# Kernel optimization log

Measured on AMD Instinct MI355X. Metric: run time of the kernel, lower is better.

Reference implementation:

```python
import jax, jax.numpy as jnp
import numpy as np

C = 768; H = 12; D = C // H; R = 8; SCALE = 0.5; EPS = 1e-12
NEG = -1e9

def _lin(x, W, b):
    return x @ W + b

def _ln(x, g, b):
    m = jnp.mean(x, axis=-1, keepdims=True)
    v = jnp.mean((x - m) ** 2, axis=-1, keepdims=True)
    return (x - m) * jax.lax.rsqrt(v + EPS) * g + b

def setup_inputs() -> dict:
    key = jax.random.key(0)
    ks = jax.random.split(key, 16)
    B, T, K = 8, 512, 4
    s = 0.02
    inp = {
        'x': jax.random.normal(ks[0], (B, T, C), jnp.float32),
        'mask': jnp.ones((B, T), jnp.int32),
        'neighbour_rep': jax.random.normal(ks[1], (B, T - 1, K, C), jnp.float32),
        'Wq': jax.random.normal(ks[2], (C, C), jnp.float32) * s,
        'bq': jnp.zeros((C,), jnp.float32),
        'Wk': jax.random.normal(ks[3], (C, C), jnp.float32) * s,
        'bk': jnp.zeros((C,), jnp.float32),
        'Wv': jax.random.normal(ks[4], (C, C), jnp.float32) * s,
        'bv': jnp.zeros((C,), jnp.float32),
        'Wp': jax.random.normal(ks[5], (C, C), jnp.float32) * s,
        'bp': jnp.zeros((C,), jnp.float32),
        'Wd': jax.random.normal(ks[6], (C, R), jnp.float32) * s,
        'bd': jnp.zeros((R,), jnp.float32),
        'Wu': jax.random.normal(ks[7], (R, C), jnp.float32) * s,
        'bu': jnp.zeros((C,), jnp.float32),
        'ln_g': jnp.ones((C,), jnp.float32),
        'ln_b': jnp.zeros((C,), jnp.float32),
    }
    return inp

def _softmax_stable(att):
    # manual max-sub-exp-sum softmax, matching stable_softmax
    att = att - jnp.max(att, axis=-1, keepdims=True)
    att = jnp.exp(att)
    return att / jnp.sum(att, axis=-1, keepdims=True)

def _heads(t, n_tok):
    B = t.shape[0]
    return t.reshape(B, n_tok, H, D)

def reference(x, mask, neighbour_rep, Wq, bq, Wk, bk, Wv, bv, Wp, bp, Wd, bd, Wu, bu, ln_g, ln_b):
    B, T, _ = x.shape
    inv = 1.0 / jnp.sqrt(jnp.float32(D))
    mvalid = (mask != 0)[:, None, None, :]  # [B,1,1,T]

    # ---- self attention: queries are x[:,1:], keys/values over full seq ----
    q = _heads(_lin(x[:, 1:], Wq, bq), T - 1)      # [B,T-1,H,D]
    k = _heads(_lin(x, Wk, bk), T)                 # [B,T,H,D]
    v = _heads(_lin(x, Wv, bv), T)
    att = jnp.einsum('bqhd,bkhd->bhqk', q, k) * inv
    att = jnp.where(mvalid, att, NEG)
    att = _softmax_stable(att)
    y_self = jnp.einsum('bhqk,bkhd->bqhd', att, v).reshape(B, T - 1, C)
    y_self = _lin(y_self, Wp, bp)

    # ---- cls attention: single query (token 0), low-rank key projection ----
    qc = _heads(_lin(x[:, :1], Wq, bq), 1)                         # [B,1,H,D]
    kc = _heads(_lin(_lin(x, Wd, bd), Wu, bu), T)                  # [B,T,H,D]
    attc = jnp.einsum('bqhd,bkhd->bhqk', qc, kc) * inv
    attc = jnp.where(mvalid, attc, NEG)
    attc = _softmax_stable(attc)
    y_cls = jnp.einsum('bhqk,bkhd->bqhd', attc, v).reshape(B, 1, C)
    y_cls = _lin(y_cls, Wp, bp)

    # ---- neighbour attention over small candidate set per token ----
    cand = jnp.concatenate([x[:, 1:, None, :], neighbour_rep], axis=2)  # [B,T-1,Kc,C]
    Kc = cand.shape[2]
    qn = _lin(cand, Wq, bq).reshape(B, T - 1, Kc, H, D)
    kn = _lin(_lin(cand, Wd, bd), Wu, bu).reshape(B, T - 1, Kc, H, D)
    vn = _lin(cand, Wv, bv).reshape(B, T - 1, Kc, H, D)
    attn = jnp.einsum('btihd,btjhd->bthij', qn, kn) * inv
    attn = _softmax_stable(attn)
    out = jnp.einsum('bthij,btjhd->btihd', attn, vn).reshape(B, T - 1, Kc, C)
    out = _lin(out, Wp, bp)
    y_neigh = out[:, :, 0, :]
    neigh_tmp = out[:, :, 1:, :]

    y = SCALE * y_neigh + (1.0 - SCALE) * y_self
    neighbour_out = _ln(neigh_tmp + neighbour_rep, ln_g, ln_b)
    y = jnp.concatenate([y_cls, y], axis=1)
    y = _ln(y + x, ln_g, ln_b)
    return y, neighbour_out
```

## Files before the change

### kernel.cpp

```cpp
#include <hip/hip_runtime.h>
#include <math.h>

#define C_    768
#define H_    12
#define D_    64
#define B_    8
#define T_    512
#define TM1   511
#define R_    8
#define KN_   4
#define KC5   5
#define SCALE_ 0.5f
#define EPS_  1e-12f
#define NEG_  -1000000000.0f
#define INV_  0.125f
#define LDQ   2560
#define QPOFF 2304
#define NT_   4096
#define NRR_  16352

typedef __bf16 bf16_t;
typedef __bf16 bf16x4_t __attribute__((ext_vector_type(4)));
typedef __bf16 bf16x8_t __attribute__((ext_vector_type(8)));
typedef float  f32x4_t  __attribute__((ext_vector_type(4)));
typedef const void __attribute__((address_space(1)))* gas_t;
typedef void       __attribute__((address_space(3)))* las_t;

__device__ __forceinline__ void gl_lds16(const bf16_t* g, bf16_t* l) {
  __builtin_amdgcn_global_load_lds((gas_t)g, (las_t)l, 16, 0, 0);
}

struct GemmDesc {
  const bf16_t* A; int lda;
  const bf16_t* Bt;
  const float* bias;
  bf16_t* Cbf; int ldc;
  bf16_t* Ctr; int trcol0; int mode;
  int M, K, N, gx, nwg;
};

__global__ __launch_bounds__(256) void prep(
    const float* __restrict__ x, const float* __restrict__ nrep,
    const float* __restrict__ Wq, const float* __restrict__ Wk,
    const float* __restrict__ Wv, const float* __restrict__ Wp,
    const float* __restrict__ Wd, const float* __restrict__ Wu,
    const float* __restrict__ bq, const float* __restrict__ bk,
    const float* __restrict__ bv, const float* __restrict__ bu,
    bf16_t* __restrict__ xbf, bf16_t* __restrict__ nrbf,
    bf16_t* __restrict__ Wbig, bf16_t* __restrict__ Wtp,
    float* __restrict__ WdT, float* __restrict__ bbig)
{
  __shared__ float tile[32][33];
  const int bid = blockIdx.x, tid = threadIdx.x;
  if (bid < 1024) {
    const long n = (long)NT_ * C_;
    for (long i = ((long)bid * 256 + tid) * 4; i < n; i += (long)1024 * 256 * 4) {
      float4 v = *(const float4*)(x + i);
      bf16x4_t o = {(bf16_t)v.x, (bf16_t)v.y, (bf16_t)v.z, (bf16_t)v.w};
      *(bf16x4_t*)(xbf + i) = o;
    }
  } else if (bid < 3072) {
    const long n = (long)NRR_ * C_;
    for (long i = ((long)(bid - 1024) * 256 + tid) * 4; i < n;
         i += (long)2048 * 256 * 4) {
      float4 v = *(const float4*)(nrep + i);
      bf16x4_t o = {(bf16_t)v.x, (bf16_t)v.y, (bf16_t)v.z, (bf16_t)v.w};
      *(bf16x4_t*)(nrbf + i) = o;
    }
  } else if (bid < 5376) {
    int sub = bid - 3072;
    const int which = sub / 576; sub %= 576;
    const float* W = which == 0 ? Wq : which == 1 ? Wk : which == 2 ? Wv : Wp;
    bf16_t* Wt = (which == 3) ? Wtp : Wbig + (size_t)which * C_ * C_;
    const int n0 = (sub % 24) * 32, k0 = (sub / 24) * 32;
    const int tx = tid & 31, ty = tid >> 5;
    #pragma unroll
    for (int r = ty; r < 32; r += 8)
      tile[r][tx] = W[(size_t)(k0 + r) * C_ + n0 + tx];
    __syncthreads();
    #pragma unroll
    for (int r = ty; r < 32; r += 8)
      Wt[(size_t)(n0 + r) * C_ + k0 + tx] = (bf16_t)tile[tx][r];
  } else if (bid < 6144) {
    const int idx = (bid - 5376) * 256 + tid;
    const int n = idx / C_, k = idx % C_;
    const int h = n >> 4, r = n & 15;
    float s = 0.f;
    if (h < H_) {
      if (r < 8) {
        #pragma unroll 8
        for (int j = 0; j < 64; ++j)
          s += Wu[r * C_ + h * 64 + j] * Wq[(size_t)k * C_ + h * 64 + j];
      } else if (r == 8) {
        #pragma unroll 8
        for (int j = 0; j < 64; ++j)
          s += bu[h * 64 + j] * Wq[(size_t)k * C_ + h * 64 + j];
      }
    }
    Wbig[(size_t)(QPOFF + n) * C_ + k] = (bf16_t)s;
  } else if (bid < 6168) {
    const int idx = (bid - 6144) * 256 + tid;
    if (idx < R_ * C_) {
      const int r = idx / C_, k = idx % C_;
      WdT[idx] = Wd[(size_t)k * R_ + r];
    }
  } else {
    const int i = (bid - 6168) * 256 + tid;
    if (i < 2560) {
      float v;
      if (i < 768) v = bq[i];
      else if (i < 1536) v = bk[i - 768];
      else if (i < 2304) v = bv[i - 1536];
      else {
        const int n = i - 2304, h = n >> 4, r = n & 15;
        v = 0.f;
        if (h < H_) {
          if (r < 8) {
            float s = 0.f;
            for (int j = 0; j < 64; ++j) s += bq[h * 64 + j] * Wu[r * C_ + h * 64 + j];
            v = s;
          } else if (r == 8) {
            float s = 0.f;
            for (int j = 0; j < 64; ++j) s += bq[h * 64 + j] * bu[h * 64 + j];
            v = s;
          }
        }
      }
      bbig[i] = v;
    }
  }
}

__device__ __forceinline__ void gemm_body(const GemmDesc& d, int bid0, char* pool)
{
  bf16_t* As = (bf16_t*)pool;
  bf16_t* Bs = (bf16_t*)(pool + 16384);
  bf16_t* Cs = (bf16_t*)pool;

  int lid = bid0;
  {
    const int nwg = d.nwg;
    const int q0 = nwg >> 3, r0 = nwg & 7;
    const int xcd = lid & 7, idx = lid >> 3;
    lid = (xcd < r0 ? xcd * (q0 + 1) : r0 * (q0 + 1) + (xcd - r0) * q0) + idx;
  }
  const int row0 = (lid / d.gx) * 128;
  const int col0 = (lid % d.gx) * 128;

  const int tid = threadIdx.x;
  const int lane = tid & 63;
  const int wv = tid >> 6;
  const int wr = (wv >> 1) * 64;
  const int wc = (wv & 1) * 64;

  const int srl = wv * 8 + (lane >> 3);
  const int scol = 8 * ((lane & 7) ^ (srl & 7));

  const bf16_t* gA[4];
  const bf16_t* gB[4];
  #pragma unroll
  for (int i = 0; i < 4; ++i) {
    int ar = row0 + i * 32 + srl; if (ar > d.M - 1) ar = d.M - 1;
    gA[i] = d.A + (size_t)ar * d.lda + scol;
    gB[i] = d.Bt + (size_t)(col0 + i * 32 + srl) * d.K + scol;
  }

  f32x4_t acc[4][4];
  #pragma unroll
  for (int i = 0; i < 4; ++i)
    #pragma unroll
    for (int j = 0; j < 4; ++j) acc[i][j] = (f32x4_t){0.f, 0.f, 0.f, 0.f};

  const int fm = lane & 15;
  const int g = lane >> 4;
  const int f7 = fm & 7;

  for (int k0 = 0; k0 < d.K; k0 += 64) {
    #pragma unroll
    for (int i = 0; i < 4; ++i)
      gl_lds16(gA[i] + k0, As + i * 2048 + wv * 512);
    #pragma unroll
    for (int i = 0; i < 4; ++i)
      gl_lds16(gB[i] + k0, Bs + i * 2048 + wv * 512);
    __syncthreads();
    #pragma unroll
    for (int h = 0; h < 2; ++h) {
      const int sl = 8 * (((h << 2) + g) ^ f7);
      bf16x8_t af[4], bfr[4];
      #pragma unroll
      for (int mi = 0; mi < 4; ++mi)
        af[mi] = *(const bf16x8_t*)(As + (wr + mi * 16 + fm) * 64 + sl);
      #pragma unroll
      for (int ni = 0; ni < 4; ++ni)
        bfr[ni] = *(const bf16x8_t*)(Bs + (wc + ni * 16 + fm) * 64 + sl);
      __builtin_amdgcn_s_setprio(1);
      #pragma unroll
      for (int mi = 0; mi < 4; ++mi)
        #pragma unroll
        for (int ni = 0; ni < 4; ++ni)
          acc[mi][ni] = __builtin_amdgcn_mfma_f32_16x16x32_bf16(af[mi], bfr[ni],
                                                                acc[mi][ni], 0, 0, 0);
      __builtin_amdgcn_s_setprio(0);
    }
    __syncthreads();
  }

  const int r4 = (lane >> 4) * 4;

  if (d.mode & 2) {
    #pragma unroll
    for (int ni = 0; ni < 4; ++ni) {
      const int col = col0 + wc + ni * 16 + fm;
      if ((unsigned)(col - d.trcol0) < 768u) {
        const int vcol = col - d.trcol0;
        const float bv = d.bias[col];
        #pragma unroll
        for (int mi = 0; mi < 4; ++mi) {
          const int rb = row0 + wr + mi * 16 + r4;
          bf16x4_t o4 = {(bf16_t)(acc[mi][ni][0] + bv), (bf16_t)(acc[mi][ni][1] + bv),
                         (bf16_t)(acc[mi][ni][2] + bv), (bf16_t)(acc[mi][ni][3] + bv)};
          size_t idx = ((size_t)(rb >> 9) * H_ + (size_t)(vcol >> 6)) * ((size_t)D_ * T_)
                     + (size_t)(vcol & 63) * T_ + (size_t)(rb & 511);
          *(bf16x4_t*)(d.Ctr + idx) = o4;
        }
      }
    }
  }

  #pragma unroll
  for (int p = 0; p < 2; ++p) {
    if (wr == p * 64) {
      #pragma unroll
      for (int ni = 0; ni < 4; ++ni) {
        const int col = wc + ni * 16 + fm;
        const float bv = d.bias[col0 + col];
        #pragma unroll
        for (int mi = 0; mi < 4; ++mi) {
          const int lrow = mi * 16 + r4;
          #pragma unroll
          for (int r = 0; r < 4; ++r)
            Cs[(lrow + r) * 136 + col] = (bf16_t)(acc[mi][ni][r] + bv);
        }
      }
    }
    __syncthreads();
    const int rrow = tid >> 2;
    const int cc = (tid & 3) * 32;
    const int grow = row0 + p * 64 + rrow;
    if ((d.mode & 1) && grow < d.M) {
      bf16_t* gp = d.Cbf + (size_t)grow * d.ldc + col0 + cc;
      const bf16_t* lp = Cs + rrow * 136 + cc;
      #pragma unroll
      for (int j = 0; j < 4; ++j)
        *(bf16x8_t*)(gp + j * 8) = *(const bf16x8_t*)(lp + j * 8);
    }
    __syncthreads();
  }
}

__device__ __forceinline__ void gemv8w_body(
    const bf16_t* __restrict__ A, const float* __restrict__ WdT,
    const float* __restrict__ bd, float* __restrict__ out, int M, int bid)
{
  const int w = (int)threadIdx.x >> 6, lane = (int)threadIdx.x & 63;
  const int row0 = bid * 16 + w * 4;
  #pragma unroll
  for (int rr = 0; rr < 4; ++rr) {
    const int row = row0 + rr;
    if (row >= M) return;
    const bf16_t* ar = A + (size_t)row * C_ + lane * 12;
    float xv[12];
    #pragma unroll
    for (int c = 0; c < 3; ++c) {
      bf16x4_t v = *(const bf16x4_t*)(ar + c * 4);
      #pragma unroll
      for (int j = 0; j < 4; ++j) xv[c * 4 + j] = (float)v[j];
    }
    float acc[8];
    #pragma unroll
    for (int r = 0; r < 8; ++r) {
      const float* wr = WdT + r * C_ + lane * 12;
      float4 w0 = *(const float4*)(wr);
      float4 w1 = *(const float4*)(wr + 4);
      float4 w2 = *(const float4*)(wr + 8);
      acc[r] = xv[0]*w0.x + xv[1]*w0.y + xv[2]*w0.z + xv[3]*w0.w
             + xv[4]*w1.x + xv[5]*w1.y + xv[6]*w1.z + xv[7]*w1.w
             + xv[8]*w2.x + xv[9]*w2.y + xv[10]*w2.z + xv[11]*w2.w;
    }
    #pragma unroll
    for (int off = 32; off > 0; off >>= 1) {
      #pragma unroll
      for (int r = 0; r < 8; ++r) acc[r] += __shfl_xor(acc[r], off);
    }
    if (lane == 0) {
      #pragma unroll
      for (int r = 0; r < 8; ++r)
        out[(size_t)row * R_ + r] = acc[r] + bd[r];
    }
  }
}

__global__ __launch_bounds__(256) void mega1(
    GemmDesc d0, int n0, GemmDesc d1, int n1,
    const bf16_t* Ag1, const bf16_t* Ag2,
    const float* WdT, const float* bd,
    float* o1, int M1, int ng1, float* o2, int M2)
{
  __shared__ __align__(16) char pool[32768];
  int bid = blockIdx.x;
  if (bid < n0) { gemm_body(d0, bid, pool); return; }
  bid -= n0;
  if (bid < n1) { gemm_body(d1, bid, pool); return; }
  bid -= n1;
  if (bid < ng1) { gemv8w_body(Ag1, WdT, bd, o1, M1, bid); return; }
  bid -= ng1;
  gemv8w_body(Ag2, WdT, bd, o2, M2, bid);
}

__global__ __launch_bounds__(256) void gemm_mfma_k(GemmDesc d) {
  __shared__ __align__(16) char pool[32768];
  gemm_body(d, blockIdx.x, pool);
}

__device__ void attn_body(
    const bf16_t* __restrict__ QKVc, const bf16_t* __restrict__ Vtg,
    const int* __restrict__ mask, bf16_t* __restrict__ yout,
    char* pool, int bid)
{
  bf16_t* Ks   = (bf16_t*)pool;
  bf16_t* Vs   = (bf16_t*)(pool + 8192);
  bf16_t* Pl   = (bf16_t*)(pool + 16384);
  float* fac_s = (float*)(pool + 24576);
  float* l_s   = (float*)(pool + 24832);
  int*   msk_s = (int*)(pool + 25088);

  const int qt0 = (bid & 7) * 64;
  const int h = (bid >> 3) % H_;
  const int b = bid / 96;
  const int tid = threadIdx.x;
  const int lane = tid & 63;
  const int w = tid >> 6;
  const int lq = lane & 15;
  const int g = lane >> 4;

  const int qi_frag = qt0 + w * 16 + lq;
  const int qtok = (qi_frag < TM1 ? qi_frag : TM1 - 1) + 1;
  bf16x8_t qf[2];
  {
    const bf16_t* qp = QKVc + ((size_t)(b * T_) + qtok) * LDQ + h * D_ + 8 * g;
    qf[0] = *(const bf16x8_t*)qp;
    qf[1] = *(const bf16x8_t*)(qp + 32);
  }

  const bf16_t* kbase = QKVc + (size_t)(b * T_) * LDQ + 768 + h * D_;
  const bf16_t* vbase = Vtg + ((size_t)(b * H_) + h) * ((size_t)D_ * T_);

  f32x4_t o[4];
  #pragma unroll
  for (int i = 0; i < 4; ++i) o[i] = (f32x4_t){0.f, 0.f, 0.f, 0.f};
  float m = -INFINITY, l = 0.f;

  for (int kt = 0; kt < T_; kt += 64) {
    #pragma unroll
    for (int i = 0; i < 2; ++i) {
      const int tp = tid + i * 256;
      const int kr = tp >> 3;
      const int sl = tp & 7;
      const int ss = sl ^ (kr & 7);
      gl_lds16(kbase + (size_t)(kt + kr) * LDQ + 8 * ss,
               Ks + (size_t)(i * 4 + w) * 512);
      gl_lds16(vbase + (size_t)kr * T_ + kt + 8 * ss,
               Vs + (size_t)(i * 4 + w) * 512);
    }
    if (tid < 64) msk_s[tid] = mask[b * T_ + kt + tid];
    __syncthreads();

    f32x4_t st[4];
    __builtin_amdgcn_s_setprio(1);
    #pragma unroll
    for (int t = 0; t < 4; ++t) {
      st[t] = (f32x4_t){0.f, 0.f, 0.f, 0.f};
      const int kk = t * 16 + lq;
      const bf16_t* krow = Ks + kk * 64;
      bf16x8_t kf0 = *(const bf16x8_t*)(krow + 8 * ((g)     ^ (kk & 7)));
      bf16x8_t kf1 = *(const bf16x8_t*)(krow + 8 * ((4 + g) ^ (kk & 7)));
      st[t] = __builtin_amdgcn_mfma_f32_16x16x32_bf16(kf0, qf[0], st[t], 0, 0, 0);
      st[t] = __builtin_amdgcn_mfma_f32_16x16x32_bf16(kf1, qf[1], st[t], 0, 0, 0);
    }
    __builtin_amdgcn_s_setprio(0);

    float p[16];
    float mt = -INFINITY;
    #pragma unroll
    for (int t = 0; t < 4; ++t) {
      const int4 mk = *(const int4*)&msk_s[t * 16 + 4 * g];
      p[4*t+0] = mk.x ? st[t][0] * INV_ : NEG_;
      p[4*t+1] = mk.y ? st[t][1] * INV_ : NEG_;
      p[4*t+2] = mk.z ? st[t][2] * INV_ : NEG_;
      p[4*t+3] = mk.w ? st[t][3] * INV_ : NEG_;
      mt = fmaxf(mt, fmaxf(fmaxf(p[4*t], p[4*t+1]), fmaxf(p[4*t+2], p[4*t+3])));
    }
    mt = fmaxf(mt, __shfl_xor(mt, 16));
    mt = fmaxf(mt, __shfl_xor(mt, 32));
    const float mnew = fmaxf(m, mt);
    const float fac = __expf(m - mnew);
    float ps = 0.f;
    #pragma unroll
    for (int i = 0; i < 16; ++i) { p[i] = __expf(p[i] - mnew); ps += p[i]; }
    ps += __shfl_xor(ps, 16);
    ps += __shfl_xor(ps, 32);
    l = l * fac + ps;
    m = mnew;
    if (lane < 16) fac_s[w * 16 + lane] = fac;

    bf16_t* prow = Pl + w * 1024 + lq * 64;
    #pragma unroll
    for (int t = 0; t < 4; ++t) {
      bf16x4_t pb = {(bf16_t)p[4*t], (bf16_t)p[4*t+1],
                     (bf16_t)p[4*t+2], (bf16_t)p[4*t+3]};
      *(bf16x4_t*)(prow + 8 * ((2*t + (g >> 1)) ^ (lq & 7)) + 4 * (g & 1)) = pb;
    }
    bf16x8_t pa0 = *(const bf16x8_t*)(prow + 8 * ((g)     ^ (lq & 7)));
    bf16x8_t pa1 = *(const bf16x8_t*)(prow + 8 * ((4 + g) ^ (lq & 7)));

    const float4 fc = *(const float4*)&fac_s[w * 16 + 4 * g];
    __builtin_amdgcn_s_setprio(1);
    #pragma unroll
    for (int db = 0; db < 4; ++db) {
      const int dr = db * 16 + lq;
      const bf16_t* vrow = Vs + dr * 64;
      bf16x8_t vf0 = *(const bf16x8_t*)(vrow + 8 * ((g)     ^ (dr & 7)));
      bf16x8_t vf1 = *(const bf16x8_t*)(vrow + 8 * ((4 + g) ^ (dr & 7)));
      o[db][0] *= fc.x; o[db][1] *= fc.y; o[db][2] *= fc.z; o[db][3] *= fc.w;
      o[db] = __builtin_amdgcn_mfma_f32_16x16x32_bf16(pa0, vf0, o[db], 0, 0, 0);
      o[db] = __builtin_amdgcn_mfma_f32_16x16x32_bf16(pa1, vf1, o[db], 0, 0, 0);
    }
    __builtin_amdgcn_s_setprio(0);
    __syncthreads();
  }

  if (lane < 16) l_s[w * 16 + lane] = l;
  const float4 lv = *(const float4*)&l_s[w * 16 + 4 * g];
  const float rl0 = 1.f / lv.x, rl1 = 1.f / lv.y;
  const float rl2 = 1.f / lv.z, rl3 = 1.f / lv.w;
  const int qr0 = qt0 + w * 16 + 4 * g;
  #pragma unroll
  for (int db = 0; db < 4; ++db) {
    const int col = h * D_ + db * 16 + lq;
    bf16_t* yp = yout + ((size_t)(b * TM1) + qr0) * C_ + col;
    if (qr0 + 0 < TM1) yp[0 * (size_t)C_] = (bf16_t)(o[db][0] * rl0);
    if (qr0 + 1 < TM1) yp[1 * (size_t)C_] = (bf16_t)(o[db][1] * rl1);
    if (qr0 + 2 < TM1) yp[2 * (size_t)C_] = (bf16_t)(o[db][2] * rl2);
    if (qr0 + 3 < TM1) yp[3 * (size_t)C_] = (bf16_t)(o[db][3] * rl3);
  }
}

__device__ void cls_body(
    const bf16_t* __restrict__ QKVc, const float* __restrict__ t1,
    const int* __restrict__ mask, float* __restrict__ yout,
    char* pool, int cbid)
{
  float* Vs   = (float*)pool;
  float* Ps   = (float*)(pool + 16640);
  float* qp_s = (float*)(pool + 16960);

  const int b = cbid / H_, h = cbid % H_;
  const int tid = threadIdx.x;
  const int lane = tid & 63;

  if (tid < 16)
    qp_s[tid] = (float)QKVc[(size_t)(b * T_) * LDQ + QPOFF + h * 16 + tid];
  __syncthreads();

  float m = -INFINITY, l = 0.f, acc = 0.f, mnew = 0.f;
  for (int kt = 0; kt < T_; kt += 64) {
    for (int rr = tid >> 6; rr < 64; rr += 4)
      Vs[rr * 65 + lane] =
          (float)QKVc[((size_t)(b * T_) + kt + rr) * LDQ + 1536 + h * D_ + lane];
    __syncthreads();
    if (tid < 64) {
      const float* t1r = t1 + ((size_t)(b * T_) + kt + tid) * R_;
      float sc = qp_s[8];
      #pragma unroll
      for (int r = 0; r < 8; ++r) sc += qp_s[r] * t1r[r];
      sc *= INV_;
      if (!mask[b * T_ + kt + tid]) sc = NEG_;
      float mt = sc;
      #pragma unroll
      for (int off = 32; off > 0; off >>= 1) mt = fmaxf(mt, __shfl_xor(mt, off));
      mnew = fmaxf(m, mt);
      float e = __expf(sc - mnew);
      float ssum = e;
      #pragma unroll
      for (int off = 32; off > 0; off >>= 1) ssum += __shfl_xor(ssum, off);
      float fac = __expf(m - mnew);
      acc *= fac;
      l = l * fac + ssum;
      Ps[tid] = e;
    }
    __syncthreads();
    if (tid < 64) {
      #pragma unroll
      for (int j = 0; j < 64; ++j) acc += Ps[j] * Vs[j * 65 + tid];
      m = mnew;
    }
    __syncthreads();
  }
  if (tid < 64) yout[(size_t)b * C_ + h * D_ + tid] = acc / l;
}

__global__ __launch_bounds__(256) void attn_cls(
    const bf16_t* __restrict__ QKVc, const bf16_t* __restrict__ Vtg,
    const int* __restrict__ mask, bf16_t* __restrict__ yout,
    const float* __restrict__ t1, float* __restrict__ ych)
{
  __shared__ __align__(16) char pool[25344];
  const int bid = blockIdx.x;
  if (bid < 768) attn_body(QKVc, Vtg, mask, yout, pool, bid);
  else           cls_body(QKVc, t1, mask, ych, pool, bid - 768);
}

__global__ __launch_bounds__(256) void neigh_clsp(
    const bf16_t* __restrict__ QKVc, const float* __restrict__ t1,
    const bf16_t* __restrict__ vqn, const float* __restrict__ t2,
    const bf16_t* __restrict__ ysh, int b0, bf16_t* __restrict__ outn,
    int nNeigh, const float* __restrict__ ych, const float* __restrict__ Wp,
    const float* __restrict__ bp, float* __restrict__ ycp)
{
  __shared__ float vs[KC5 * C_];
  __shared__ float qp_s[KC5][200];
  __shared__ float t2_s[KC5][8];
  __shared__ float Ps[H_ * 25];
  __shared__ float as_[C_];

  const int tid = threadIdx.x;
  int bid = blockIdx.x;
  if (bid >= nNeigh) {
    const int cbid = bid - nNeigh;
    const int row = cbid / 3;
    const int c = (cbid % 3) * 256 + tid;
    for (int i = tid; i < C_; i += 256) as_[i] = ych[(size_t)row * C_ + i];
    __syncthreads();
    float acc = bp[c];
    for (int k = 0; k < C_; ++k) acc += as_[k] * Wp[(size_t)k * C_ + c];
    ycp[(size_t)row * C_ + c] = acc;
    return;
  }

  const int bt = bid;
  const int bb = bt / TM1, t = bt % TM1;
  const int b = b0 + bb;
  const size_t tok = (size_t)(b * T_) + t + 1;
  const size_t nrow = ((size_t)(bb * TM1) + t) * KN_;

  for (int idx = tid; idx < KC5 * 96; idx += 256) {
    int i = idx / 96, d8 = (idx % 96) * 8;
    const bf16_t* vp = (i == 0) ? QKVc + tok * LDQ + 1536 + d8
                                : vqn + (nrow + i - 1) * 1024 + d8;
    bf16x8_t vv = *(const bf16x8_t*)vp;
    #pragma unroll
    for (int j = 0; j < 8; ++j) vs[i * C_ + d8 + j] = (float)vv[j];
  }
  for (int idx = tid; idx < KC5 * 24; idx += 256) {
    int i = idx / 24, c8 = (idx % 24) * 8;
    const bf16_t* qpp = (i == 0) ? QKVc + tok * LDQ + QPOFF + c8
                                 : vqn + (nrow + i - 1) * 1024 + 768 + c8;
    bf16x8_t qv = *(const bf16x8_t*)qpp;
    #pragma unroll
    for (int j = 0; j < 8; ++j) qp_s[i][c8 + j] = (float)qv[j];
  }
  if (tid < KC5 * 8) {
    int i = tid / 8, r = tid & 7;
    t2_s[i][r] = (i == 0) ? t1[tok * R_ + r] : t2[(nrow + i - 1) * R_ + r];
  }
  __syncthreads();

  if (tid < H_ * KC5) {
    int h = tid / KC5, i = tid % KC5;
    float sc[KC5];
    #pragma unroll
    for (int j = 0; j < KC5; ++j) {
      float s = qp_s[i][h * 16 + 8];
      #pragma unroll
      for (int r = 0; r < 8; ++r) s += qp_s[i][h * 16 + r] * t2_s[j][r];
      sc[j] = s * INV_;
    }
    float mt = sc[0];
    #pragma unroll
    for (int j = 1; j < KC5; ++j) mt = fmaxf(mt, sc[j]);
    float e[KC5], ssum = 0.f;
    #pragma unroll
    for (int j = 0; j < KC5; ++j) { e[j] = __expf(sc[j] - mt); ssum += e[j]; }
    float rs = 1.f / ssum;
    #pragma unroll
    for (int j = 0; j < KC5; ++j) Ps[h * 25 + i * KC5 + j] = e[j] * rs;
  }
  __syncthreads();

  const bf16_t* ysrow = ysh + ((size_t)(b * TM1) + t) * C_;
  for (int idx = tid; idx < KC5 * C_; idx += 256) {
    int i = idx / C_, c = idx % C_;
    int h = c / D_;
    float sum = 0.f;
    #pragma unroll
    for (int j = 0; j < KC5; ++j)
      sum += Ps[h * 25 + i * KC5 + j] * vs[j * C_ + c];
    if (i == 0) sum = SCALE_ * sum + (1.f - SCALE_) * (float)ysrow[c];
    outn[(((size_t)(bb * TM1) + t) * KC5 + i) * C_ + c] = (bf16_t)sum;
  }
}

__device__ __forceinline__ void block_reduce2(float& s, float& ss, float* red) {
  #pragma unroll
  for (int off = 32; off > 0; off >>= 1) {
    s += __shfl_down(s, off);
    ss += __shfl_down(ss, off);
  }
  int wid = threadIdx.x >> 6;
  if ((threadIdx.x & 63) == 0) { red[wid * 2] = s; red[wid * 2 + 1] = ss; }
  __syncthreads();
  s  = red[0] + red[2] + red[4] + red[6];
  ss = red[1] + red[3] + red[5] + red[7];
}

__device__ __forceinline__ void ln_row(const float vals[3], float s, float ss,
                                       const float* __restrict__ g,
                                       const float* __restrict__ bb,
                                       float* __restrict__ orow, float* red) {
  block_reduce2(s, ss, red);
  float mean = s * (1.f / (float)C_);
  float var = ss * (1.f / (float)C_) - mean * mean;
  var = fmaxf(var, 0.f);
  float rs = rsqrtf(var + EPS_);
  #pragma unroll
  for (int ii = 0; ii < 3; ++ii) {
    int c = threadIdx.x + ii * 256;
    orow[c] = (vals[ii] - mean) * rs * g[c] + bb[c];
  }
}

__global__ __launch_bounds__(256) void combine_all(
    const bf16_t* __restrict__ poutnb, const float* __restrict__ x,
    const float* __restrict__ g, const float* __restrict__ bln,
    int b0, float* __restrict__ dout, float* __restrict__ dout1,
    const bf16_t* __restrict__ nrcbf, int nMain,
    const float* __restrict__ ycp, int withCls)
{
  __shared__ float red[8];
  int bid = blockIdx.x;
  float vals[3], s = 0.f, ss = 0.f;
  if (bid < nMain) {
    const int bbb = bid / TM1, t = bid % TM1;
    const int b = b0 + bbb;
    const bf16_t* pn = poutnb + (((size_t)(bbb * TM1) + t) * KC5 + 0) * C_;
    const float* xr = x + ((size_t)(b * T_) + t + 1) * C_;
    float* orow = dout + ((size_t)(b * T_) + t + 1) * C_;
    #pragma unroll
    for (int ii = 0; ii < 3; ++ii) {
      int c = threadIdx.x + ii * 256;
      float v = (float)pn[c] + xr[c];
      vals[ii] = v; s += v; ss += v * v;
    }
    ln_row(vals, s, ss, g, bln, orow, red);
    return;
  }
  bid -= nMain;
  if (bid < nMain * KN_) {
    const int i1 = bid % KN_;
    const int bt = bid / KN_;
    const int bbb = bt / TM1, t = bt % TM1;
    const int b = b0 + bbb;
    const bf16_t* pn = poutnb + ((size_t)bt * KC5 + 1 + i1) * C_;
    const bf16_t* nr = nrcbf + ((size_t)bt * KN_ + i1) * C_;
    float* orow = dout1 + (((size_t)(b * TM1) + t) * KN_ + i1) * C_;
    #pragma unroll
    for (int ii = 0; ii < 3; ++ii) {
      int c = threadIdx.x + ii * 256;
      float v = (float)pn[c] + (float)nr[c];
      vals[ii] = v; s += v; ss += v * v;
    }
    ln_row(vals, s, ss, g, bln, orow, red);
    return;
  }
  bid -= nMain * KN_;
  (void)withCls;
  const int b = bid;
  const float* yc = ycp + (size_t)b * C_;
  const float* xr = x + (size_t)(b * T_) * C_;
  float* orow = dout + (size_t)(b * T_) * C_;
  #pragma unroll
  for (int ii = 0; ii < 3; ++ii) {
    int c = threadIdx.x + ii * 256;
    float v = yc[c] + xr[c];
    vals[ii] = v; s += v; ss += v * v;
  }
  ln_row(vals, s, ss, g, bln, orow, red);
}

extern "C" void kernel_launch(void* const* d_in, const int* in_sizes, int n_in,
                              void* d_out, int out_size, void* d_ws, size_t ws_size,
                              hipStream_t stream) {
  (void)in_sizes; (void)n_in; (void)out_size;
  const float* x    = (const float*)d_in[0];
  const int*   mask = (const int*)d_in[1];
  const float* nrep = (const float*)d_in[2];
  const float* Wq = (const float*)d_in[3];  const float* bq = (const float*)d_in[4];
  const float* Wk = (const float*)d_in[5];  const float* bk = (const float*)d_in[6];
  const float* Wv = (const float*)d_in[7];  const float* bv = (const float*)d_in[8];
  const float* Wp = (const float*)d_in[9];  const float* bp = (const float*)d_in[10];
  const float* Wd = (const float*)d_in[11]; const float* bd = (const float*)d_in[12];
  const float* Wu = (const float*)d_in[13]; const float* bu = (const float*)d_in[14];
  const float* lng = (const float*)d_in[15];
  const float* lnb = (const float*)d_in[16];
  float* dout = (float*)d_out;
  const size_t OUT1 = (size_t)B_ * T_ * C_;

  char* ws = (char*)d_ws;
  size_t off = 0;
  auto alloc = [&](size_t bytes) -> void* {
    void* p = ws + off; off += (bytes + 255) & ~(size_t)255; return p;
  };
  const size_t NT = (size_t)NT_;
  const size_t NR = (size_t)NRR_;
  const size_t YSROWS = (size_t)B_ * TM1;

  bf16_t* xbf   = (bf16_t*)alloc(NT * C_ * 2);
  bf16_t* nrbf  = (bf16_t*)alloc(NR * C_ * 2);
  bf16_t* Wbig  = (bf16_t*)alloc((size_t)2560 * C_ * 2);
  bf16_t* Wtp   = (bf16_t*)alloc((size_t)C_ * C_ * 2);
  float*  WdT   = (float*)alloc((size_t)R_ * C_ * 4);
  float*  bbig  = (float*)alloc(2560 * 4);
  bf16_t* QKVc  = (bf16_t*)alloc(NT * LDQ * 2);
  bf16_t* Vtg   = (bf16_t*)alloc(NT * C_ * 2);
  float*  t1    = (float*)alloc(NT * R_ * 4);
  bf16_t* ysh   = (bf16_t*)alloc(YSROWS * C_ * 2);
  float*  ych   = (float*)alloc((size_t)B_ * C_ * 4);
  float*  ycp   = (float*)alloc((size_t)B_ * C_ * 4);
  const size_t fixed = off;
  const size_t perb = (size_t)TM1 * KN_ * 1024 * 2
                    + (size_t)TM1 * KN_ * R_ * 4
                    + (size_t)TM1 * KC5 * C_ * 2 * 2 + 5 * 256;
  int nb = 1;
  for (int cand : {8, 4, 2, 1}) {
    if (fixed + perb * (size_t)cand <= ws_size) { nb = cand; break; }
  }
  bf16_t* outn   = (bf16_t*)alloc((size_t)nb * TM1 * KC5 * C_ * 2);
  bf16_t* poutnb = (bf16_t*)alloc((size_t)nb * TM1 * KC5 * C_ * 2);
  bf16_t* vqn  = (bf16_t*)alloc((size_t)nb * TM1 * KN_ * 1024 * 2);
  float*  t2   = (float*)alloc((size_t)nb * TM1 * KN_ * R_ * 4);

  dim3 blk(256);

  prep<<<6178, blk, 0, stream>>>(x, nrep, Wq, Wk, Wv, Wp, Wd, Wu,
                                 bq, bk, bv, bu,
                                 xbf, nrbf, Wbig, Wtp, WdT, bbig);

  GemmDesc dqkv;
  dqkv.A = xbf; dqkv.lda = C_; dqkv.Bt = Wbig; dqkv.bias = bbig;
  dqkv.Cbf = QKVc; dqkv.ldc = LDQ; dqkv.Ctr = Vtg; dqkv.trcol0 = 1536;
  dqkv.mode = 3; dqkv.M = (int)NT; dqkv.K = C_; dqkv.N = 2560;
  dqkv.gx = 20; dqkv.nwg = 640;

  bool first = true;
  for (int b0 = 0; b0 < B_; b0 += nb) {
    const int Mn = nb * TM1 * KN_;
    const int Mo = nb * TM1 * KC5;
    const bf16_t* nrcbf = nrbf + (size_t)b0 * TM1 * KN_ * C_;

    GemmDesc dvqn;
    dvqn.A = nrcbf; dvqn.lda = C_; dvqn.Bt = Wbig + (size_t)1536 * C_;
    dvqn.bias = bbig + 1536; dvqn.Cbf = vqn; dvqn.ldc = 1024;
    dvqn.Ctr = nullptr; dvqn.trcol0 = 0; dvqn.mode = 1;
    dvqn.M = Mn; dvqn.K = C_; dvqn.N = 1024;
    dvqn.gx = 8; dvqn.nwg = 8 * ((Mn + 127) / 128);

    const int n0 = first ? 640 : 0;
    const int M1 = first ? (int)NT : 0;
    const int ng1 = first ? (int)((NT + 15) / 16) : 0;
    const int ng2 = (Mn + 15) / 16;

    mega1<<<n0 + dvqn.nwg + ng1 + ng2, blk, 0, stream>>>(
        dqkv, n0, dvqn, dvqn.nwg, xbf, nrcbf, WdT, bd, t1, M1, ng1, t2, Mn);

    if (first) {
      attn_cls<<<768 + 96, blk, 0, stream>>>(QKVc, Vtg, mask, ysh, t1, ych);
    }

    neigh_clsp<<<nb * TM1 + (first ? 24 : 0), blk, 0, stream>>>(
        QKVc, t1, vqn, t2, ysh, b0, outn, nb * TM1, ych, Wp, bp, ycp);

    GemmDesc dproj;
    dproj.A = outn; dproj.lda = C_; dproj.Bt = Wtp; dproj.bias = bp;
    dproj.Cbf = poutnb; dproj.ldc = C_; dproj.Ctr = nullptr; dproj.trcol0 = 0;
    dproj.mode = 1; dproj.M = Mo; dproj.K = C_; dproj.N = C_;
    dproj.gx = 6; dproj.nwg = 6 * ((Mo + 127) / 128);
    gemm_mfma_k<<<dproj.nwg, blk, 0, stream>>>(dproj);

    combine_all<<<nb * TM1 * (1 + KN_) + (first ? 8 : 0), blk, 0, stream>>>(
        poutnb, x, lng, lnb, b0, dout, dout + OUT1, nrcbf, nb * TM1,
        ycp, first ? 1 : 0);

    first = false;
  }
}
```

Measured before the change: 248.6 us.

## Fold output projection into value weights to drop the post-attention projection GEMM

Precomputes Wv·Wp (and bv·Wp+bp) with a small GEMM so the V projection produces already-projected values. Since softmax rows sum to one, attention over projected values equals projecting the attention output, so the separate neighbour projection GEMM and the cls projection blocks are removed. This saves a large M×768×768 GEMM per batch chunk and one intermediate buffer, at the cost of an extra 768³ weight GEMM and bf16 rounding of the fused weights.

```diff
diff --git a/kernel.cpp b/kernel.cpp
--- a/kernel.cpp
+++ b/kernel.cpp
@@ -46,9 +46,12 @@
     const float* __restrict__ Wd, const float* __restrict__ Wu,
     const float* __restrict__ bq, const float* __restrict__ bk,
     const float* __restrict__ bv, const float* __restrict__ bu,
+    const float* __restrict__ bp,
     bf16_t* __restrict__ xbf, bf16_t* __restrict__ nrbf,
     bf16_t* __restrict__ Wbig, bf16_t* __restrict__ Wtp,
-    float* __restrict__ WdT, float* __restrict__ bbig)
+    bf16_t* __restrict__ Wvbf,
+    float* __restrict__ WdT, float* __restrict__ bbig,
+    float* __restrict__ zb768)
 {
   __shared__ float tile[32][33];
   const int bid = blockIdx.x, tid = threadIdx.x;
@@ -70,17 +73,24 @@
   } else if (bid < 5376) {
     int sub = bid - 3072;
     const int which = sub / 576; sub %= 576;
-    const float* W = which == 0 ? Wq : which == 1 ? Wk : which == 2 ? Wv : Wp;
-    bf16_t* Wt = (which == 3) ? Wtp : Wbig + (size_t)which * C_ * C_;
-    const int n0 = (sub % 24) * 32, k0 = (sub / 24) * 32;
-    const int tx = tid & 31, ty = tid >> 5;
-    #pragma unroll
-    for (int r = ty; r < 32; r += 8)
-      tile[r][tx] = W[(size_t)(k0 + r) * C_ + n0 + tx];
-    __syncthreads();
-    #pragma unroll
-    for (int r = ty; r < 32; r += 8)
-      Wt[(size_t)(n0 + r) * C_ + k0 + tx] = (bf16_t)tile[tx][r];
+    if (which == 2) {
+      const long i = ((long)sub * 256 + tid) * 4;
+      float4 v = *(const float4*)(Wv + i);
+      bf16x4_t o = {(bf16_t)v.x, (bf16_t)v.y, (bf16_t)v.z, (bf16_t)v.w};
+      *(bf16x4_t*)(Wvbf + i) = o;
+    } else {
+      const float* W = which == 0 ? Wq : which == 1 ? Wk : Wp;
+      bf16_t* Wt = (which == 3) ? Wtp : Wbig + (size_t)which * C_ * C_;
+      const int n0 = (sub % 24) * 32, k0 = (sub / 24) * 32;
+      const int tx = tid & 31, ty = tid >> 5;
+      #pragma unroll
+      for (int r = ty; r < 32; r += 8)
+        tile[r][tx] = W[(size_t)(k0 + r) * C_ + n0 + tx];
+      __syncthreads();
+      #pragma unroll
+      for (int r = ty; r < 32; r += 8)
+        Wt[(size_t)(n0 + r) * C_ + k0 + tx] = (bf16_t)tile[tx][r];
+    }
   } else if (bid < 6144) {
     const int idx = (bid - 5376) * 256 + tid;
     const int n = idx / C_, k = idx % C_;
@@ -110,8 +120,12 @@
       float v;
       if (i < 768) v = bq[i];
       else if (i < 1536) v = bk[i - 768];
-      else if (i < 2304) v = bv[i - 1536];
-      else {
+      else if (i < 2304) {
+        const int n = i - 1536;
+        float s = bp[n];
+        for (int m = 0; m < C_; ++m) s += bv[m] * Wp[(size_t)m * C_ + n];
+        v = s;
+      } else {
         const int n = i - 2304, h = n >> 4, r = n & 15;
         v = 0.f;
         if (h < H_) {
@@ -127,6 +141,8 @@
         }
       }
       bbig[i] = v;
+    } else if (i < 3328) {
+      zb768[i - 2560] = 0.f;
     }
   }
 }
@@ -457,7 +473,7 @@
 
 __device__ void cls_body(
     const bf16_t* __restrict__ QKVc, const float* __restrict__ t1,
-    const int* __restrict__ mask, float* __restrict__ yout,
+    const int* __restrict__ mask, float* __restrict__ ycp,
     char* pool, int cbid)
 {
   float* Vs   = (float*)pool;
@@ -506,48 +522,32 @@
     }
     __syncthreads();
   }
-  if (tid < 64) yout[(size_t)b * C_ + h * D_ + tid] = acc / l;
+  if (tid < 64) ycp[(size_t)b * C_ + h * D_ + tid] = acc / l;
 }
 
 __global__ __launch_bounds__(256) void attn_cls(
     const bf16_t* __restrict__ QKVc, const bf16_t* __restrict__ Vtg,
     const int* __restrict__ mask, bf16_t* __restrict__ yout,
-    const float* __restrict__ t1, float* __restrict__ ych)
+    const float* __restrict__ t1, float* __restrict__ ycp)
 {
   __shared__ __align__(16) char pool[25344];
   const int bid = blockIdx.x;
   if (bid < 768) attn_body(QKVc, Vtg, mask, yout, pool, bid);
-  else           cls_body(QKVc, t1, mask, ych, pool, bid - 768);
-}
-
-__global__ __launch_bounds__(256) void neigh_clsp(
+  else           cls_body(QKVc, t1, mask, ycp, pool, bid - 768);
+}
+
+__global__ __launch_bounds__(256) void neigh_attn(
     const bf16_t* __restrict__ QKVc, const float* __restrict__ t1,
     const bf16_t* __restrict__ vqn, const float* __restrict__ t2,
-    const bf16_t* __restrict__ ysh, int b0, bf16_t* __restrict__ outn,
-    int nNeigh, const float* __restrict__ ych, const float* __restrict__ Wp,
-    const float* __restrict__ bp, float* __restrict__ ycp)
+    const bf16_t* __restrict__ ysp, int b0, bf16_t* __restrict__ poutn)
 {
   __shared__ float vs[KC5 * C_];
   __shared__ float qp_s[KC5][200];
   __shared__ float t2_s[KC5][8];
   __shared__ float Ps[H_ * 25];
-  __shared__ float as_[C_];
 
   const int tid = threadIdx.x;
-  int bid = blockIdx.x;
-  if (bid >= nNeigh) {
-    const int cbid = bid - nNeigh;
-    const int row = cbid / 3;
-    const int c = (cbid % 3) * 256 + tid;
-    for (int i = tid; i < C_; i += 256) as_[i] = ych[(size_t)row * C_ + i];
-    __syncthreads();
-    float acc = bp[c];
-    for (int k = 0; k < C_; ++k) acc += as_[k] * Wp[(size_t)k * C_ + c];
-    ycp[(size_t)row * C_ + c] = acc;
-    return;
-  }
-
-  const int bt = bid;
+  const int bt = blockIdx.x;
   const int bb = bt / TM1, t = bt % TM1;
   const int b = b0 + bb;
   const size_t tok = (size_t)(b * T_) + t + 1;
@@ -597,7 +597,7 @@
   }
   __syncthreads();
 
-  const bf16_t* ysrow = ysh + ((size_t)(b * TM1) + t) * C_;
+  const bf16_t* ysrow = ysp + ((size_t)(b * TM1) + t) * C_;
   for (int idx = tid; idx < KC5 * C_; idx += 256) {
     int i = idx / C_, c = idx % C_;
     int h = c / D_;
@@ -606,7 +606,7 @@
     for (int j = 0; j < KC5; ++j)
       sum += Ps[h * 25 + i * KC5 + j] * vs[j * C_ + c];
     if (i == 0) sum = SCALE_ * sum + (1.f - SCALE_) * (float)ysrow[c];
-    outn[(((size_t)(bb * TM1) + t) * KC5 + i) * C_ + c] = (bf16_t)sum;
+    poutn[(((size_t)(bb * TM1) + t) * KC5 + i) * C_ + c] = (bf16_t)sum;
   }
 }
 
@@ -728,32 +728,39 @@
   bf16_t* nrbf  = (bf16_t*)alloc(NR * C_ * 2);
   bf16_t* Wbig  = (bf16_t*)alloc((size_t)2560 * C_ * 2);
   bf16_t* Wtp   = (bf16_t*)alloc((size_t)C_ * C_ * 2);
+  bf16_t* Wvbf  = (bf16_t*)alloc((size_t)C_ * C_ * 2);
   float*  WdT   = (float*)alloc((size_t)R_ * C_ * 4);
   float*  bbig  = (float*)alloc(2560 * 4);
+  float*  zb768 = (float*)alloc(768 * 4);
   bf16_t* QKVc  = (bf16_t*)alloc(NT * LDQ * 2);
   bf16_t* Vtg   = (bf16_t*)alloc(NT * C_ * 2);
   float*  t1    = (float*)alloc(NT * R_ * 4);
-  bf16_t* ysh   = (bf16_t*)alloc(YSROWS * C_ * 2);
-  float*  ych   = (float*)alloc((size_t)B_ * C_ * 4);
+  bf16_t* ysp   = (bf16_t*)alloc(YSROWS * C_ * 2);
   float*  ycp   = (float*)alloc((size_t)B_ * C_ * 4);
   const size_t fixed = off;
   const size_t perb = (size_t)TM1 * KN_ * 1024 * 2
                     + (size_t)TM1 * KN_ * R_ * 4
-                    + (size_t)TM1 * KC5 * C_ * 2 * 2 + 5 * 256;
+                    + (size_t)TM1 * KC5 * C_ * 2 + 4 * 256;
   int nb = 1;
   for (int cand : {8, 4, 2, 1}) {
     if (fixed + perb * (size_t)cand <= ws_size) { nb = cand; break; }
   }
-  bf16_t* outn   = (bf16_t*)alloc((size_t)nb * TM1 * KC5 * C_ * 2);
   bf16_t* poutnb = (bf16_t*)alloc((size_t)nb * TM1 * KC5 * C_ * 2);
   bf16_t* vqn  = (bf16_t*)alloc((size_t)nb * TM1 * KN_ * 1024 * 2);
   float*  t2   = (float*)alloc((size_t)nb * TM1 * KN_ * R_ * 4);
 
   dim3 blk(256);
 
-  prep<<<6178, blk, 0, stream>>>(x, nrep, Wq, Wk, Wv, Wp, Wd, Wu,
-                                 bq, bk, bv, bu,
-                                 xbf, nrbf, Wbig, Wtp, WdT, bbig);
+  prep<<<6181, blk, 0, stream>>>(x, nrep, Wq, Wk, Wv, Wp, Wd, Wu,
+                                 bq, bk, bv, bu, bp,
+                                 xbf, nrbf, Wbig, Wtp, Wvbf, WdT, bbig, zb768);
+
+  GemmDesc dwvp;
+  dwvp.A = Wtp; dwvp.lda = C_; dwvp.Bt = Wvbf; dwvp.bias = zb768;
+  dwvp.Cbf = Wbig + (size_t)1536 * C_; dwvp.ldc = C_;
+  dwvp.Ctr = nullptr; dwvp.trcol0 = 0; dwvp.mode = 1;
+  dwvp.M = C_; dwvp.K = C_; dwvp.N = C_; dwvp.gx = 6; dwvp.nwg = 36;
+  gemm_mfma_k<<<36, blk, 0, stream>>>(dwvp);
 
   GemmDesc dqkv;
   dqkv.A = xbf; dqkv.lda = C_; dqkv.Bt = Wbig; dqkv.bias = bbig;
@@ -764,7 +771,6 @@
   bool first = true;
   for (int b0 = 0; b0 < B_; b0 += nb) {
     const int Mn = nb * TM1 * KN_;
-    const int Mo = nb * TM1 * KC5;
     const bf16_t* nrcbf = nrbf + (size_t)b0 * TM1 * KN_ * C_;
 
     GemmDesc dvqn;
@@ -783,18 +789,10 @@
         dqkv, n0, dvqn, dvqn.nwg, xbf, nrcbf, WdT, bd, t1, M1, ng1, t2, Mn);
 
     if (first) {
-      attn_cls<<<768 + 96, blk, 0, stream>>>(QKVc, Vtg, mask, ysh, t1, ych);
-    }
-
-    neigh_clsp<<<nb * TM1 + (first ? 24 : 0), blk, 0, stream>>>(
-        QKVc, t1, vqn, t2, ysh, b0, outn, nb * TM1, ych, Wp, bp, ycp);
-
-    GemmDesc dproj;
-    dproj.A = outn; dproj.lda = C_; dproj.Bt = Wtp; dproj.bias = bp;
-    dproj.Cbf = poutnb; dproj.ldc = C_; dproj.Ctr = nullptr; dproj.trcol0 = 0;
-    dproj.mode = 1; dproj.M = Mo; dproj.K = C_; dproj.N = C_;
-    dproj.gx = 6; dproj.nwg = 6 * ((Mo + 127) / 128);
-    gemm_mfma_k<<<dproj.nwg, blk, 0, stream>>>(dproj);
+      attn_cls<<<768 + 96, blk, 0, stream>>>(QKVc, Vtg, mask, ysp, t1, ycp);
+    }
+
+    neigh_attn<<<nb * TM1, blk, 0, stream>>>(QKVc, t1, vqn, t2, ysp, b0, poutnb);
 
     combine_all<<<nb * TM1 * (1 + KN_) + (first ? 8 : 0), blk, 0, stream>>>(
         poutnb, x, lng, lnb, b0, dout, dout + OUT1, nrcbf, nb * TM1,
```

New measurement: 242.7 us. -2.4%, faster.
